# Performance work log

Hardware: AMD Instinct MI355X
Metric: run time of the kernel (lower is better)

## Reference

```python
import jax, jax.numpy as jnp
import numpy as np

D_MODEL = 1024
N_HEADS = 16
HEAD_DIM = D_MODEL // N_HEADS
EPS = 1e-6


def setup_inputs() -> dict:
    key = jax.random.key(0)
    ks = jax.random.split(key, 10)
    s = 0.02
    return {
        "sequence": jax.random.normal(ks[0], (4, 2048, D_MODEL), dtype=jnp.float32),
        "ln_gamma": jnp.ones((D_MODEL,), jnp.float32),
        "ln_beta": jnp.zeros((D_MODEL,), jnp.float32),
        "Wq": jax.random.normal(ks[1], (D_MODEL, D_MODEL), jnp.float32) * s,
        "bq": jnp.zeros((D_MODEL,), jnp.float32),
        "Wk": jax.random.normal(ks[2], (D_MODEL, D_MODEL), jnp.float32) * s,
        "bk": jnp.zeros((D_MODEL,), jnp.float32),
        "Wv": jax.random.normal(ks[3], (D_MODEL, D_MODEL), jnp.float32) * s,
        "bv": jnp.zeros((D_MODEL,), jnp.float32),
        "Wo": jax.random.normal(ks[4], (D_MODEL, D_MODEL), jnp.float32) * s,
        "bo": jnp.zeros((D_MODEL,), jnp.float32),
        "mu": jnp.zeros((1, 1, 1, 1), jnp.float32),
    }


def _split_heads(x):
    b, s, d = x.shape
    return x.reshape(b, s, N_HEADS, HEAD_DIM).transpose(0, 2, 1, 3)  # [B,H,S,hd]


def reference(sequence, ln_gamma, ln_beta, Wq, bq, Wk, bk, Wv, bv, Wo, bo, mu):
    # LayerNorm (eps=1e-6)
    mean = jnp.mean(sequence, axis=-1, keepdims=True)
    var = jnp.mean(jnp.square(sequence - mean), axis=-1, keepdims=True)
    x = (sequence - mean) / jnp.sqrt(var + EPS) * ln_gamma + ln_beta

    # QKV projections (torch Linear: x @ W.T + b)
    q = _split_heads(x @ Wq.T + bq)
    k = _split_heads(x @ Wk.T + bk)
    v = _split_heads(x @ Wv.T + bv)

    scale = HEAD_DIM ** 0.5
    scores = jnp.einsum("bhqd,bhkd->bhqk", q, k) / scale  # [B,H,S,S]
    scores = jax.nn.sigmoid(scores - mu) * jnp.exp(scores)
    scores = scores / jnp.sum(scores, axis=-1, keepdims=True)

    out = jnp.einsum("bhqk,bhkd->bhqd", scores, v)  # [B,H,S,hd]
    b, h, s, hd = out.shape
    out = out.transpose(0, 2, 1, 3).reshape(b, s, h * hd)
    return out @ Wo.T + bo  # dropout is identity at inference
```

## Files before the change

kernel.cpp:

```cpp
#include <hip/hip_runtime.h>
#include <hip/hip_bf16.h>
#include <cstdint>
#include <cstddef>


typedef __bf16 bf16_t;
typedef __bf16 bf16x4 __attribute__((ext_vector_type(4)));
typedef __bf16 bf16x8 __attribute__((ext_vector_type(8)));
typedef float  f32x4  __attribute__((ext_vector_type(4)));

#define MFMA16(a, b, c) __builtin_amdgcn_mfma_f32_16x16x32_bf16((a), (b), (c), 0, 0, 0)

#if __has_builtin(__builtin_amdgcn_exp2f)
#define VEXP2(x) __builtin_amdgcn_exp2f(x)
#else
#define VEXP2(x) __expf((x) * 0.6931471805599453f)
#endif

__device__ __forceinline__ void gload16(void* lds, const void* g) {
  __builtin_amdgcn_global_load_lds(
      (__attribute__((address_space(1))) void*)(uintptr_t)g,
      (__attribute__((address_space(3))) void*)(uint32_t)(uintptr_t)lds,
      16, 0, 0);
}

__global__ __launch_bounds__(256) void cvt_w_k(
    const float* __restrict__ s0, const float* __restrict__ s1,
    const float* __restrict__ s2, const float* __restrict__ s3,
    bf16_t* __restrict__ dst)
{
  const float* src = blockIdx.y == 0 ? s0 : blockIdx.y == 1 ? s1
                   : blockIdx.y == 2 ? s2 : s3;
  int i = blockIdx.x * 256 + threadIdx.x;
  float4 v = ((const float4*)src)[i];
  bf16x4 o = { (bf16_t)v.x, (bf16_t)v.y, (bf16_t)v.z, (bf16_t)v.w };
  *(bf16x4*)(dst + (((size_t)blockIdx.y) << 20) + (size_t)i * 4) = o;
}

__global__ __launch_bounds__(256) void ln_k(
    const float* __restrict__ x, const float* __restrict__ gamma,
    const float* __restrict__ beta, bf16_t* __restrict__ out)
{
  int row = blockIdx.x;
  int tid = threadIdx.x;
  float4 v = ((const float4*)(x + (size_t)row * 1024))[tid];
  float s  = v.x + v.y + v.z + v.w;
  float ss = v.x * v.x + v.y * v.y + v.z * v.z + v.w * v.w;
#pragma unroll
  for (int m = 1; m < 64; m <<= 1) { s += __shfl_xor(s, m); ss += __shfl_xor(ss, m); }
  __shared__ float sh_s[4], sh_q[4];
  int w = tid >> 6;
  if ((tid & 63) == 0) { sh_s[w] = s; sh_q[w] = ss; }
  __syncthreads();
  s  = sh_s[0] + sh_s[1] + sh_s[2] + sh_s[3];
  ss = sh_q[0] + sh_q[1] + sh_q[2] + sh_q[3];
  float mean = s * (1.0f / 1024.0f);
  float var  = ss * (1.0f / 1024.0f) - mean * mean;
  float rstd = rsqrtf(var + 1e-6f);
  float4 gv = ((const float4*)gamma)[tid];
  float4 bv = ((const float4*)beta)[tid];
  bf16x4 o = { (bf16_t)((v.x - mean) * rstd * gv.x + bv.x),
               (bf16_t)((v.y - mean) * rstd * gv.y + bv.y),
               (bf16_t)((v.z - mean) * rstd * gv.z + bv.z),
               (bf16_t)((v.w - mean) * rstd * gv.w + bv.w) };
  *(bf16x4*)(out + (size_t)row * 1024 + tid * 4) = o;
}

__global__ __launch_bounds__(256) void gemm_bt(
    const bf16_t* __restrict__ A, const bf16_t* __restrict__ Bw,
    const float* __restrict__ b0, const float* __restrict__ b1,
    const float* __restrict__ b2,
    void* __restrict__ o0, void* __restrict__ o1, void* __restrict__ o2,
    int M, int N, int K, int fused)
{
  __shared__ __align__(16) bf16_t a_lds[2][128][32];
  __shared__ __align__(16) bf16_t b_lds[2][128][32];
  const int tid = threadIdx.x;
  const int l = tid & 63, w = tid >> 6;
  const int wr = w >> 1, wc = w & 1;
  const int m0 = blockIdx.y * 128, n0 = blockIdx.x * 128;
  const int lr = l & 15, lg = l >> 4;

  f32x4 acc[4][4] = {};

  const int srow = tid >> 2;
  const int scol = (tid & 3) * 8;
  const bf16_t* ag = A  + (size_t)(m0 + srow) * K + scol;
  const bf16_t* bg = Bw + (size_t)(n0 + srow) * K + scol;

  gload16((char*)a_lds[0] + tid * 16,        ag);
  gload16((char*)a_lds[0] + 4096 + tid * 16, ag + (size_t)64 * K);
  gload16((char*)b_lds[0] + tid * 16,        bg);
  gload16((char*)b_lds[0] + 4096 + tid * 16, bg + (size_t)64 * K);
  __syncthreads();

  int cur = 0;
  for (int k0 = 0; k0 < K; k0 += 32) {
    if (k0 + 32 < K) {
      gload16((char*)a_lds[cur ^ 1] + tid * 16,        ag + k0 + 32);
      gload16((char*)a_lds[cur ^ 1] + 4096 + tid * 16, ag + (size_t)64 * K + k0 + 32);
      gload16((char*)b_lds[cur ^ 1] + tid * 16,        bg + k0 + 32);
      gload16((char*)b_lds[cur ^ 1] + 4096 + tid * 16, bg + (size_t)64 * K + k0 + 32);
    }
    bf16x8 af[4], bf[4];
#pragma unroll
    for (int i = 0; i < 4; ++i) {
      af[i] = *(const bf16x8*)&a_lds[cur][wr * 64 + i * 16 + lr][lg * 8];
      bf[i] = *(const bf16x8*)&b_lds[cur][wc * 64 + i * 16 + lr][lg * 8];
    }
#pragma unroll
    for (int i = 0; i < 4; ++i)
#pragma unroll
      for (int j = 0; j < 4; ++j)
        acc[i][j] = MFMA16(af[i], bf[j], acc[i][j]);
    __syncthreads();
    cur ^= 1;
  }

  int matsel = fused ? (n0 >> 10) : 0;
  const float* bias = matsel == 0 ? b0 : matsel == 1 ? b1 : b2;
  float bs[4];
#pragma unroll
  for (int j = 0; j < 4; ++j) bs[j] = bias[(n0 + wc * 64 + j * 16 + lr) & 1023];

#pragma unroll
  for (int i = 0; i < 4; ++i) {
#pragma unroll
    for (int j = 0; j < 4; ++j) {
#pragma unroll
      for (int r = 0; r < 4; ++r) {
        int row = m0 + wr * 64 + i * 16 + lg * 4 + r;
        int col = n0 + wc * 64 + j * 16 + lr;
        float v = acc[i][j][r] + bs[j];
        if (!fused) {
          ((float*)o0)[(size_t)row * N + col] = v;
        } else {
          int nn = col & 1023;
          int bb = row >> 11, s = row & 2047, hh = nn >> 6, d = nn & 63;
          if (matsel == 2) {
            ((bf16_t*)o2)[((((size_t)bb * 16 + hh) * 64) + d) * 2048 + s] = (bf16_t)v;
          } else {
            bf16_t* o = matsel ? (bf16_t*)o1 : (bf16_t*)o0;
            if (matsel == 0) v *= 0.18033688011112042f;
            o[((((size_t)bb * 16 + hh) * 2048 + s) << 6) + d] = (bf16_t)v;
          }
        }
      }
    }
  }
}

__global__ __launch_bounds__(256) void attn_k(
    const bf16_t* __restrict__ q, const bf16_t* __restrict__ k,
    const bf16_t* __restrict__ vT, const float* __restrict__ mu_p,
    bf16_t* __restrict__ out)
{
  const int S = 2048;
  int hw = blockIdx.x;
  int vid = (hw & 7) * 128 + (hw >> 3);
  int qt = vid & 15;
  int bh = vid >> 4;
  int h = bh & 15, b = bh >> 4;

  const bf16_t* qb = q  + ((size_t)bh * S + qt * 128) * 64;
  const char* kbase = (const char*)(k  + (size_t)bh * S * 64);
  const char* vbase = (const char*)(vT + (size_t)bh * 64 * S);
  const float emu = __expf(mu_p[0]);

  __shared__ __align__(16) bf16_t k_lds[2][64][64];
  __shared__ __align__(16) bf16_t v_lds[2][64][64];
  __shared__ __align__(16) bf16_t p_lds[4][16][64];

  const int tid = threadIdx.x, l = tid & 63, w = tid >> 6;
  const int lr = l & 15, lg = l >> 4;
  const int swz = (lr & 7) << 4;

  bf16x8 qa[2][2];
#pragma unroll
  for (int sub = 0; sub < 2; ++sub)
#pragma unroll
    for (int ch = 0; ch < 2; ++ch)
      qa[sub][ch] = *(const bf16x8*)(qb + (size_t)(w * 32 + sub * 16 + lr) * 64
                                     + ch * 32 + lg * 8);

  const int srow = tid >> 3;
  const int ssw  = ((tid & 7) * 16) ^ ((srow & 7) << 4);
  const int koff = srow * 128 + ssw;
  const int voff = srow * 4096 + ssw;

  f32x4 o[2][4] = {};
  f32x4 rsum4[2] = {};

#pragma unroll
  for (int c = 0; c < 2; ++c) {
    gload16((char*)k_lds[0] + c * 4096 + tid * 16, kbase + koff + c * 4096);
    gload16((char*)v_lds[0] + c * 4096 + tid * 16, vbase + voff + c * 131072);
  }
  __syncthreads();

  char* pbase = (char*)p_lds[w];
#pragma unroll 2
  for (int t = 0; t < 32; ++t) {
    const int cur = t & 1;
    if (t + 1 < 32) {
#pragma unroll
      for (int c = 0; c < 2; ++c) {
        gload16((char*)k_lds[cur ^ 1] + c * 4096 + tid * 16,
                kbase + koff + c * 4096 + (t + 1) * 8192);
        gload16((char*)v_lds[cur ^ 1] + c * 4096 + tid * 16,
                vbase + voff + c * 131072 + (t + 1) * 128);
      }
    }

    bf16x8 kf[4][2];
#pragma unroll
    for (int cc = 0; cc < 4; ++cc)
#pragma unroll
      for (int ch = 0; ch < 2; ++ch)
        kf[cc][ch] = *(const bf16x8*)((const char*)k_lds[cur]
                       + (cc * 16 + lr) * 128 + ((ch * 64 + lg * 16) ^ swz));

#pragma unroll
    for (int sub = 0; sub < 2; ++sub) {
      f32x4 sc4[4];
#pragma unroll
      for (int cc = 0; cc < 4; ++cc) {
        f32x4 a = {};
        a = MFMA16(kf[cc][0], qa[sub][0], a);
        a = MFMA16(kf[cc][1], qa[sub][1], a);
        sc4[cc] = a;
      }
#pragma unroll
      for (int cc = 0; cc < 4; ++cc) {
        bf16x4 pw;
        f32x4 wv;
#pragma unroll
        for (int r = 0; r < 4; ++r) {
          float e = VEXP2(sc4[cc][r]);
          float wgt = e * e * __builtin_amdgcn_rcpf(e + emu);
          wv[r] = wgt;
          pw[r] = (bf16_t)wgt;
        }
        rsum4[sub] += wv;
        *(bf16x4*)(pbase + lr * 128 + ((cc * 32 + lg * 8) ^ swz)) = pw;
      }
      bf16x8 pa0 = *(const bf16x8*)(pbase + lr * 128 + ((lg * 16) ^ swz));
      bf16x8 pa1 = *(const bf16x8*)(pbase + lr * 128 + ((64 + lg * 16) ^ swz));
#pragma unroll
      for (int cc = 0; cc < 4; ++cc) {
        bf16x8 vf0 = *(const bf16x8*)((const char*)v_lds[cur]
                       + (cc * 16 + lr) * 128 + ((lg * 16) ^ swz));
        bf16x8 vf1 = *(const bf16x8*)((const char*)v_lds[cur]
                       + (cc * 16 + lr) * 128 + ((64 + lg * 16) ^ swz));
        o[sub][cc] = MFMA16(pa0, vf0, o[sub][cc]);
        o[sub][cc] = MFMA16(pa1, vf1, o[sub][cc]);
      }
    }
    __syncthreads();
  }

#pragma unroll
  for (int sub = 0; sub < 2; ++sub) {
    float rs = (rsum4[sub][0] + rsum4[sub][1]) + (rsum4[sub][2] + rsum4[sub][3]);
    rs += __shfl_xor(rs, 16);
    rs += __shfl_xor(rs, 32);
    float rinv = __builtin_amdgcn_rcpf(rs);
    float ro[4];
#pragma unroll
    for (int r = 0; r < 4; ++r) {
      int src = (l & 48) | ((4 * lg + r) & 15);
      ro[r] = __shfl(rinv, src);
    }
#pragma unroll
    for (int cc = 0; cc < 4; ++cc)
#pragma unroll
      for (int r = 0; r < 4; ++r) {
        int srow_g = qt * 128 + w * 32 + sub * 16 + 4 * lg + r;
        int col = h * 64 + cc * 16 + lr;
        out[((size_t)b * 2048 + srow_g) * 1024 + col] = (bf16_t)(o[sub][cc][r] * ro[r]);
      }
  }
}

extern "C" void kernel_launch(void* const* d_in, const int* in_sizes, int n_in,
                              void* d_out, int out_size, void* d_ws, size_t ws_size,
                              hipStream_t stream) {
  const float* seq = (const float*)d_in[0];
  const float* g   = (const float*)d_in[1];
  const float* be  = (const float*)d_in[2];
  const float* Wq  = (const float*)d_in[3];
  const float* bq  = (const float*)d_in[4];
  const float* Wk  = (const float*)d_in[5];
  const float* bk  = (const float*)d_in[6];
  const float* Wv  = (const float*)d_in[7];
  const float* bv  = (const float*)d_in[8];
  const float* Wo  = (const float*)d_in[9];
  const float* bo  = (const float*)d_in[10];
  const float* mu  = (const float*)d_in[11];

  char* ws = (char*)d_ws;
  bf16_t* xb   = (bf16_t*)ws;  ws += (size_t)8192 * 1024 * 2;
  bf16_t* wAll = (bf16_t*)ws;  ws += (size_t)4 * 1024 * 1024 * 2;
  bf16_t* qb   = (bf16_t*)ws;  ws += (size_t)8192 * 1024 * 2;
  bf16_t* kbuf = (bf16_t*)ws;  ws += (size_t)8192 * 1024 * 2;
  bf16_t* vtb  = (bf16_t*)ws;  ws += (size_t)8192 * 1024 * 2;
  bf16_t* ab   = (bf16_t*)ws;  ws += (size_t)8192 * 1024 * 2;
  bf16_t* wqkv = wAll;
  bf16_t* wob  = wAll + (size_t)3 * 1024 * 1024;

  dim3 blk(256);
  cvt_w_k<<<dim3(1024, 4), blk, 0, stream>>>(Wq, Wk, Wv, Wo, wAll);
  ln_k<<<dim3(8192), blk, 0, stream>>>(seq, g, be, xb);
  gemm_bt<<<dim3(24, 64), blk, 0, stream>>>(xb, wqkv, bq, bk, bv,
                                            qb, kbuf, vtb, 8192, 3072, 1024, 1);
  attn_k<<<dim3(1024), blk, 0, stream>>>(qb, kbuf, vtb, mu, ab);
  gemm_bt<<<dim3(8, 64), blk, 0, stream>>>(ab, wob, bo, nullptr, nullptr,
                                           d_out, nullptr, nullptr, 8192, 1024, 1024, 0);
}
```

Measured before the change: 242.3 us.

## Switch attention core to 32x32 MFMA with register-resident P via permlane swap

Rewrites the attention inner loop to use 32x32x16 bf16 MFMAs. The probability tile now stays in registers, using packed bf16 conversion and v_permlane32_swap to reshape it into an A operand, which removes the per-wave LDS round trip for P. It also replaces the hardware reciprocal with a bit-trick plus two Newton iterations. The changes aim to cut LDS traffic and instruction count, at the cost of more accumulator registers and a different reciprocal accuracy profile.

Measured after the change: 271.2 us. 11.9% more time.

```diff
diff --git a/kernel.cpp b/kernel.cpp
--- a/kernel.cpp
+++ b/kernel.cpp
@@ -8,14 +8,34 @@
 typedef __bf16 bf16x4 __attribute__((ext_vector_type(4)));
 typedef __bf16 bf16x8 __attribute__((ext_vector_type(8)));
 typedef float  f32x4  __attribute__((ext_vector_type(4)));
+typedef float  f32x16 __attribute__((ext_vector_type(16)));
+typedef unsigned u32x4 __attribute__((ext_vector_type(4)));
 
 #define MFMA16(a, b, c) __builtin_amdgcn_mfma_f32_16x16x32_bf16((a), (b), (c), 0, 0, 0)
+#define MFMA32(a, b, c) __builtin_amdgcn_mfma_f32_32x32x16_bf16((a), (b), (c), 0, 0, 0)
 
 #if __has_builtin(__builtin_amdgcn_exp2f)
 #define VEXP2(x) __builtin_amdgcn_exp2f(x)
 #else
 #define VEXP2(x) __expf((x) * 0.6931471805599453f)
 #endif
+
+__device__ __forceinline__ float fast_rcp(float x) {
+  float y = __builtin_bit_cast(float, 0x7EF311C3u - __builtin_bit_cast(unsigned, x));
+  y = y * (2.0f - x * y);
+  y = y * (2.0f - x * y);
+  return y;
+}
+
+__device__ __forceinline__ unsigned cvtpk_bf16(float a, float b) {
+  unsigned r;
+  asm("v_cvt_pk_bf16_f32 %0, %1, %2" : "=v"(r) : "v"(a), "v"(b));
+  return r;
+}
+
+__device__ __forceinline__ void plane32_swap(unsigned& a, unsigned& b) {
+  asm volatile("v_permlane32_swap_b32 %0, %1" : "+v"(a), "+v"(b));
+}
 
 __device__ __forceinline__ void gload16(void* lds, const void* g) {
   __builtin_amdgcn_global_load_lds(
@@ -169,27 +189,23 @@
 
   __shared__ __align__(16) bf16_t k_lds[2][64][64];
   __shared__ __align__(16) bf16_t v_lds[2][64][64];
-  __shared__ __align__(16) bf16_t p_lds[4][16][64];
 
   const int tid = threadIdx.x, l = tid & 63, w = tid >> 6;
-  const int lr = l & 15, lg = l >> 4;
-  const int swz = (lr & 7) << 4;
-
-  bf16x8 qa[2][2];
-#pragma unroll
-  for (int sub = 0; sub < 2; ++sub)
-#pragma unroll
-    for (int ch = 0; ch < 2; ++ch)
-      qa[sub][ch] = *(const bf16x8*)(qb + (size_t)(w * 32 + sub * 16 + lr) * 64
-                                     + ch * 32 + lg * 8);
+  const int l31 = l & 31, hi = l >> 5;
+  const int swzr = (l31 & 7) << 4;
+
+  bf16x8 qf[4];
+#pragma unroll
+  for (int ch = 0; ch < 4; ++ch)
+    qf[ch] = *(const bf16x8*)(qb + (size_t)(w * 32 + l31) * 64 + ch * 16 + hi * 8);
 
   const int srow = tid >> 3;
   const int ssw  = ((tid & 7) * 16) ^ ((srow & 7) << 4);
   const int koff = srow * 128 + ssw;
   const int voff = srow * 4096 + ssw;
 
-  f32x4 o[2][4] = {};
-  f32x4 rsum4[2] = {};
+  f32x16 oAcc[2] = {};
+  float rp0 = 0.f, rp1 = 0.f, rp2 = 0.f, rp3 = 0.f;
 
 #pragma unroll
   for (int c = 0; c < 2; ++c) {
@@ -198,7 +214,6 @@
   }
   __syncthreads();
 
-  char* pbase = (char*)p_lds[w];
 #pragma unroll 2
   for (int t = 0; t < 32; ++t) {
     const int cur = t & 1;
@@ -212,73 +227,58 @@
       }
     }
 
-    bf16x8 kf[4][2];
-#pragma unroll
-    for (int cc = 0; cc < 4; ++cc)
-#pragma unroll
-      for (int ch = 0; ch < 2; ++ch)
-        kf[cc][ch] = *(const bf16x8*)((const char*)k_lds[cur]
-                       + (cc * 16 + lr) * 128 + ((ch * 64 + lg * 16) ^ swz));
-
-#pragma unroll
-    for (int sub = 0; sub < 2; ++sub) {
-      f32x4 sc4[4];
-#pragma unroll
-      for (int cc = 0; cc < 4; ++cc) {
-        f32x4 a = {};
-        a = MFMA16(kf[cc][0], qa[sub][0], a);
-        a = MFMA16(kf[cc][1], qa[sub][1], a);
-        sc4[cc] = a;
-      }
-#pragma unroll
-      for (int cc = 0; cc < 4; ++cc) {
-        bf16x4 pw;
-        f32x4 wv;
-#pragma unroll
-        for (int r = 0; r < 4; ++r) {
-          float e = VEXP2(sc4[cc][r]);
-          float wgt = e * e * __builtin_amdgcn_rcpf(e + emu);
-          wv[r] = wgt;
-          pw[r] = (bf16_t)wgt;
+#pragma unroll
+    for (int kh = 0; kh < 2; ++kh) {
+      f32x16 sc = {};
+#pragma unroll
+      for (int ch = 0; ch < 4; ++ch) {
+        bf16x8 kf = *(const bf16x8*)((const char*)k_lds[cur]
+                      + (kh * 32 + l31) * 128 + ((ch * 32 + hi * 16) ^ swzr));
+        sc = MFMA32(kf, qf[ch], sc);
+      }
+      unsigned U[8];
+#pragma unroll
+      for (int m = 0; m < 8; ++m) {
+        float e0 = VEXP2(sc[2 * m]);
+        float e1 = VEXP2(sc[2 * m + 1]);
+        float w0 = e0 * e0 * fast_rcp(e0 + emu);
+        float w1 = e1 * e1 * fast_rcp(e1 + emu);
+        rp0 += w0; rp1 += w1;
+        U[m] = cvtpk_bf16(w0, w1);
+      }
+      plane32_swap(U[0], U[2]);
+      plane32_swap(U[1], U[3]);
+      plane32_swap(U[4], U[6]);
+      plane32_swap(U[5], U[7]);
+#pragma unroll
+      for (int cc = 0; cc < 2; ++cc) {
+        u32x4 uu = { U[cc * 4 + 0], U[cc * 4 + 1], U[cc * 4 + 2], U[cc * 4 + 3] };
+        bf16x8 pa = __builtin_bit_cast(bf16x8, uu);
+        int kcol = (kh * 2 + cc) * 32 + hi * 16;
+#pragma unroll
+        for (int df = 0; df < 2; ++df) {
+          bf16x8 vf = *(const bf16x8*)((const char*)v_lds[cur]
+                        + (df * 32 + l31) * 128 + (kcol ^ swzr));
+          oAcc[df] = MFMA32(pa, vf, oAcc[df]);
         }
-        rsum4[sub] += wv;
-        *(bf16x4*)(pbase + lr * 128 + ((cc * 32 + lg * 8) ^ swz)) = pw;
-      }
-      bf16x8 pa0 = *(const bf16x8*)(pbase + lr * 128 + ((lg * 16) ^ swz));
-      bf16x8 pa1 = *(const bf16x8*)(pbase + lr * 128 + ((64 + lg * 16) ^ swz));
-#pragma unroll
-      for (int cc = 0; cc < 4; ++cc) {
-        bf16x8 vf0 = *(const bf16x8*)((const char*)v_lds[cur]
-                       + (cc * 16 + lr) * 128 + ((lg * 16) ^ swz));
-        bf16x8 vf1 = *(const bf16x8*)((const char*)v_lds[cur]
-                       + (cc * 16 + lr) * 128 + ((64 + lg * 16) ^ swz));
-        o[sub][cc] = MFMA16(pa0, vf0, o[sub][cc]);
-        o[sub][cc] = MFMA16(pa1, vf1, o[sub][cc]);
       }
     }
     __syncthreads();
   }
 
-#pragma unroll
-  for (int sub = 0; sub < 2; ++sub) {
-    float rs = (rsum4[sub][0] + rsum4[sub][1]) + (rsum4[sub][2] + rsum4[sub][3]);
-    rs += __shfl_xor(rs, 16);
-    rs += __shfl_xor(rs, 32);
-    float rinv = __builtin_amdgcn_rcpf(rs);
-    float ro[4];
-#pragma unroll
-    for (int r = 0; r < 4; ++r) {
-      int src = (l & 48) | ((4 * lg + r) & 15);
-      ro[r] = __shfl(rinv, src);
-    }
-#pragma unroll
-    for (int cc = 0; cc < 4; ++cc)
-#pragma unroll
-      for (int r = 0; r < 4; ++r) {
-        int srow_g = qt * 128 + w * 32 + sub * 16 + 4 * lg + r;
-        int col = h * 64 + cc * 16 + lr;
-        out[((size_t)b * 2048 + srow_g) * 1024 + col] = (bf16_t)(o[sub][cc][r] * ro[r]);
-      }
+  float rs = (rp0 + rp1) + (rp2 + rp3);
+  rs += __shfl_xor(rs, 32);
+  float rinv = __builtin_amdgcn_rcpf(rs);
+
+#pragma unroll
+  for (int r = 0; r < 16; ++r) {
+    int q_loc = (r & 3) + 8 * (r >> 2) + 4 * hi;
+    float ro = __shfl(rinv, q_loc);
+    size_t row = (size_t)b * 2048 + qt * 128 + w * 32 + q_loc;
+#pragma unroll
+    for (int df = 0; df < 2; ++df) {
+      out[row * 1024 + h * 64 + df * 32 + l31] = (bf16_t)(oAcc[df][r] * ro);
+    }
   }
 }
 
```
